# Performance work log

Hardware: AMD Instinct MI355X
Metric: run time of the kernel (lower is better)

## Reference

```python
import jax, jax.numpy as jnp
import numpy as np

B, T, C = 2, 2048, 1024
NUM_HEADS, QK_LEN, V_LEN = 16, 64, 64


def setup_inputs() -> dict:
    key = jax.random.key(0)
    ks = jax.random.split(key, 11)
    s = 0.02
    return {
        "Q": jax.random.normal(ks[0], (B, T, C), jnp.float32),
        "K": jax.random.normal(ks[1], (B, T, C), jnp.float32),
        "V": jax.random.normal(ks[2], (B, T, C), jnp.float32),
        # Linear weights stored as (in, out); y = x @ W + b
        "Wq": jax.random.normal(ks[3], (C, NUM_HEADS * QK_LEN), jnp.float32) * s,
        "bq": jnp.zeros((NUM_HEADS * QK_LEN,), jnp.float32),
        "Wk": jax.random.normal(ks[4], (C, NUM_HEADS * QK_LEN), jnp.float32) * s,
        "bk": jnp.zeros((NUM_HEADS * QK_LEN,), jnp.float32),
        "Wv": jax.random.normal(ks[5], (C, NUM_HEADS * V_LEN), jnp.float32) * s,
        "bv": jnp.zeros((NUM_HEADS * V_LEN,), jnp.float32),
        "Wo": jax.random.normal(ks[6], (NUM_HEADS * V_LEN, C), jnp.float32) * s,
        "bo": jnp.zeros((C,), jnp.float32),
    }


def _split_heads(x, n_heads, d):
    b, t, _ = x.shape
    return x.reshape(b, t, n_heads, d).transpose(0, 2, 1, 3)  # (B,H,T,d)


def reference(Q, K, V, Wq, bq, Wk, bk, Wv, bv, Wo, bo):
    q = _split_heads(Q @ Wq + bq, NUM_HEADS, QK_LEN)   # (B,H,T,dk)
    k = _split_heads(K @ Wk + bk, NUM_HEADS, QK_LEN)   # (B,H,T,dk)
    v = _split_heads(V @ Wv + bv, NUM_HEADS, V_LEN)    # (B,H,T,dv)

    scale = 1.0 / jnp.sqrt(jnp.asarray(QK_LEN, q.dtype))
    scores = jnp.einsum("bhqd,bhkd->bhqk", q, k) * scale  # (B,H,T,T)
    attn = jax.nn.softmax(scores, axis=-1)
    out = jnp.einsum("bhqk,bhkd->bhqd", attn, v)           # (B,H,T,dv)

    out = out.transpose(0, 2, 1, 3).reshape(Q.shape[0], Q.shape[1], NUM_HEADS * V_LEN)
    return out @ Wo + bo
```

## Files before the change

kernel.cpp:

```cpp
#include <hip/hip_runtime.h>
#include <hip/hip_bf16.h>
#include <math.h>

constexpr int B = 2, T = 2048, C = 1024, H = 16, D = 64;
constexpr int M = B * T;
constexpr float SCALE_L2E = 0.125f * 1.4426950408889634f;

typedef __attribute__((ext_vector_type(8))) short s16x8;
typedef __attribute__((ext_vector_type(4))) short s16x4;
typedef __attribute__((ext_vector_type(4))) float fv4;

typedef unsigned short ushort_t;

static __device__ __forceinline__ ushort_t f2bf(float x) {
    union { float f; unsigned u; } c; c.f = x;
    unsigned u = c.u + 0x7FFFu + ((c.u >> 16) & 1u);
    return (ushort_t)(u >> 16);
}

static __device__ __forceinline__ int cvt_pk_bf16(float lo, float hi) {
    int r;
    asm("v_cvt_pk_bf16_f32 %0, %1, %2" : "=v"(r) : "v"(lo), "v"(hi));
    return r;
}

#define GLDS(gp, lp) __builtin_amdgcn_global_load_lds( \
    (const __attribute__((address_space(1))) void*)(gp), \
    (__attribute__((address_space(3))) void*)(lp), 16, 0, 0)

__global__ __launch_bounds__(256) void prep(
    const float* __restrict__ Q, const float* __restrict__ K,
    const float* __restrict__ V,
    const float* __restrict__ W0, const float* __restrict__ W1,
    const float* __restrict__ W2, const float* __restrict__ W3,
    ushort_t* __restrict__ dst, ushort_t* __restrict__ Wt)
{
    __shared__ ushort_t tile[64][72];
    const int tid = threadIdx.x;

    if (blockIdx.x < 6144) {
        size_t e = ((size_t)blockIdx.x * 256 + tid) * 8;
        const float* src;
        size_t base;
        if (e < (size_t)M * C)          { src = Q; base = 0; }
        else if (e < 2 * (size_t)M * C) { src = K; base = (size_t)M * C; }
        else                            { src = V; base = 2 * (size_t)M * C; }
        const float* p = src + (e - base);
        float4 a = *(const float4*)p;
        float4 b = *(const float4*)(p + 4);
        union { s16x8 v; int i[4]; } o;
        o.i[0] = cvt_pk_bf16(a.x, a.y);
        o.i[1] = cvt_pk_bf16(a.z, a.w);
        o.i[2] = cvt_pk_bf16(b.x, b.y);
        o.i[3] = cvt_pk_bf16(b.z, b.w);
        *(s16x8*)(dst + e) = o.v;
        return;
    }

    const int idx = blockIdx.x - 6144;
    const int s = idx >> 8;
    const float* W = (s == 0) ? W0 : (s == 1) ? W1 : (s == 2) ? W2 : W3;
    const int k0 = (idx & 15) * 64, n0 = ((idx >> 4) & 15) * 64;
#pragma unroll
    for (int it = 0; it < 4; it++) {
        int f = it * 256 + tid;
        int r = f >> 4, c4 = (f & 15) * 4;
        float4 x = *(const float4*)(W + (size_t)(k0 + r) * C + n0 + c4);
        *(int*)&tile[r][c4]     = cvt_pk_bf16(x.x, x.y);
        *(int*)&tile[r][c4 + 2] = cvt_pk_bf16(x.z, x.w);
    }
    __syncthreads();
#pragma unroll
    for (int it = 0; it < 4; it++) {
        int f = it * 256 + tid;
        int rr = f >> 4, c4 = (f & 15) * 4;
        union { s16x4 v; ushort_t u[4]; } u;
#pragma unroll
        for (int j = 0; j < 4; j++) u.u[j] = tile[c4 + j][rr];
        *(s16x4*)(Wt + (size_t)(s * 1024 + n0 + rr) * 1024 + k0 + c4) = u.v;
    }
}

__global__ __launch_bounds__(256) void gemm_qkv(
    const ushort_t* __restrict__ qkv, const ushort_t* __restrict__ Wt,
    const float* __restrict__ bq, const float* __restrict__ bk,
    const float* __restrict__ bv,
    ushort_t* __restrict__ qw, ushort_t* __restrict__ kw,
    ushort_t* __restrict__ vt)
{
    __shared__ ushort_t As[2][128 * 32];
    __shared__ ushort_t Bs[2][128 * 32];

    const int tid = threadIdx.x;
    const int w = tid >> 6, lane = tid & 63;
    const int quad = lane >> 4, lc = lane & 15;
    const int wm = w & 1, wn = w >> 1;

    const int nt = blockIdx.x;
    const int m0 = blockIdx.y * 128;
    const int s = nt >> 3;
    const int nsec0 = (nt & 7) * 128;

    const ushort_t* Abase = qkv + (size_t)s * M * C;
    const ushort_t* Btbase = Wt + (size_t)nt * 128 * 1024;

    const int srow = (w << 4) + (lane >> 2);
    const int ske  = (lane & 3) * 8;

    fv4 acc[4][4] = {};

    auto stage = [&](int k0, int buf) {
#pragma unroll
        for (int i = 0; i < 2; i++) {
            int row = i * 64 + srow;
            GLDS(Abase + (size_t)(m0 + row) * 1024 + k0 + ske,
                 As[buf] + i * 2048 + w * 512);
            GLDS(Btbase + (size_t)row * 1024 + k0 + ske,
                 Bs[buf] + i * 2048 + w * 512);
        }
    };

    stage(0, 0);
    __syncthreads();

    for (int k0 = 0; k0 < 1024; k0 += 32) {
        const int cur = (k0 >> 5) & 1;
        if (k0 + 32 < 1024) stage(k0 + 32, cur ^ 1);

        s16x8 af[4], bf[4];
#pragma unroll
        for (int ms = 0; ms < 4; ms++)
            af[ms] = *(const s16x8*)(As[cur] + (wm * 64 + ms * 16 + lc) * 32 + quad * 8);
#pragma unroll
        for (int ns = 0; ns < 4; ns++)
            bf[ns] = *(const s16x8*)(Bs[cur] + (wn * 64 + ns * 16 + lc) * 32 + quad * 8);
#pragma unroll
        for (int ms = 0; ms < 4; ms++)
#pragma unroll
            for (int ns = 0; ns < 4; ns++)
                acc[ms][ns] = __builtin_amdgcn_mfma_f32_16x16x32_bf16(
                    af[ms], bf[ns], acc[ms][ns], 0, 0, 0);
        __syncthreads();
    }

    if (s == 2) {
#pragma unroll
        for (int ns = 0; ns < 4; ns++) {
            const int nl = nsec0 + wn * 64 + ns * 16 + lc;
            const float bias = bv[nl];
            const int h_ = nl >> 6, d_ = nl & 63;
#pragma unroll
            for (int ms = 0; ms < 4; ms++) {
                int m = m0 + wm * 64 + ms * 16 + quad * 4;
                int b_ = m >> 11, t_ = m & (T - 1);
                size_t row = (size_t)(b_ * H + h_) * 64 + d_;
                union { s16x4 v; int i[2]; } u;
                u.i[0] = cvt_pk_bf16(acc[ms][ns][0] + bias, acc[ms][ns][1] + bias);
                u.i[1] = cvt_pk_bf16(acc[ms][ns][2] + bias, acc[ms][ns][3] + bias);
                *(s16x4*)(vt + row * T + t_) = u.v;
            }
        }
        return;
    }

    const float* biasp = (s == 0) ? bq : bk;
    const float premul = (s == 0) ? SCALE_L2E : 1.0f;
    ushort_t* outp = (s == 0) ? qw : kw;

#pragma unroll
    for (int ns = 0; ns < 4; ns++) {
        const int nl = nsec0 + wn * 64 + ns * 16 + lc;
        const float bias = biasp[nl];
        const int h_ = nl >> 6, d_ = nl & 63;
#pragma unroll
        for (int ms = 0; ms < 4; ms++) {
#pragma unroll
            for (int r = 0; r < 4; r++) {
                int m = m0 + wm * 64 + ms * 16 + quad * 4 + r;
                float val = (acc[ms][ns][r] + bias) * premul;
                int b_ = m >> 11, t_ = m & (T - 1);
                size_t bh = (size_t)(b_ * H + h_);
                outp[((bh * T + t_) << 6) + d_] = f2bf(val);
            }
        }
    }
}

__global__ __launch_bounds__(256) void gemm_final(
    const ushort_t* __restrict__ A, const ushort_t* __restrict__ Wot,
    const float* __restrict__ bo, float* __restrict__ out)
{
    __shared__ ushort_t As[2][128 * 32];
    __shared__ ushort_t Bs[2][64 * 32];

    const int tid = threadIdx.x;
    const int w = tid >> 6, lane = tid & 63;
    const int quad = lane >> 4, lc = lane & 15;
    const int wm = w & 1, wn = w >> 1;

    const int n0 = blockIdx.x * 64;
    const int m0 = blockIdx.y * 128;

    const int srow = (w << 4) + (lane >> 2);
    const int ske  = (lane & 3) * 8;

    fv4 acc[4][2] = {};

    auto stage = [&](int k0, int buf) {
        GLDS(A + (size_t)(m0 + srow) * 1024 + k0 + ske,      As[buf] + w * 512);
        GLDS(A + (size_t)(m0 + 64 + srow) * 1024 + k0 + ske, As[buf] + 2048 + w * 512);
        GLDS(Wot + (size_t)(n0 + srow) * 1024 + k0 + ske,    Bs[buf] + w * 512);
    };

    stage(0, 0);
    __syncthreads();

    for (int k0 = 0; k0 < 1024; k0 += 32) {
        const int cur = (k0 >> 5) & 1;
        if (k0 + 32 < 1024) stage(k0 + 32, cur ^ 1);

        s16x8 af[4], bf[2];
#pragma unroll
        for (int ms = 0; ms < 4; ms++)
            af[ms] = *(const s16x8*)(As[cur] + (wm * 64 + ms * 16 + lc) * 32 + quad * 8);
#pragma unroll
        for (int ns = 0; ns < 2; ns++)
            bf[ns] = *(const s16x8*)(Bs[cur] + (wn * 32 + ns * 16 + lc) * 32 + quad * 8);
#pragma unroll
        for (int ms = 0; ms < 4; ms++)
#pragma unroll
            for (int ns = 0; ns < 2; ns++)
                acc[ms][ns] = __builtin_amdgcn_mfma_f32_16x16x32_bf16(
                    af[ms], bf[ns], acc[ms][ns], 0, 0, 0);
        __syncthreads();
    }

#pragma unroll
    for (int ns = 0; ns < 2; ns++) {
        const int n = n0 + wn * 32 + ns * 16 + lc;
        const float bias = bo[n];
#pragma unroll
        for (int ms = 0; ms < 4; ms++) {
#pragma unroll
            for (int r = 0; r < 4; r++) {
                int m = m0 + wm * 64 + ms * 16 + quad * 4 + r;
                out[(size_t)m * 1024 + n] = acc[ms][ns][r] + bias;
            }
        }
    }
}

__global__ __launch_bounds__(256, 4) void attn(
    const ushort_t* __restrict__ q, const ushort_t* __restrict__ k,
    const ushort_t* __restrict__ vT, ushort_t* __restrict__ o)
{
    __shared__ alignas(16) ushort_t ks[2][64 * 64];
    __shared__ alignas(16) ushort_t vs[2][64 * 64];

    const int tid = threadIdx.x;
    const int w = tid >> 6, lane = tid & 63;
    const int quad = lane >> 4, lc = lane & 15;
    const int cs = lc & 7;
    const int qsub = w & 1, ksub = w >> 1;

    const int id = blockIdx.y * 32 + blockIdx.x;
    const int qt = (id >> 3) & 31;
    const int bh = (id & 7) * 4 + (id >> 8);

    s16x8 aq[2][2];
    const ushort_t* qb = q + ((size_t)bh * T + qt * 64 + qsub * 32) * D;
#pragma unroll
    for (int j = 0; j < 2; j++)
#pragma unroll
        for (int h = 0; h < 2; h++)
            aq[j][h] = *(const s16x8*)(qb + (size_t)(j * 16 + lc) * D + h * 32 + quad * 8);

    fv4 accO[2][4] = {};
    float psum[2] = {0.f, 0.f};

    const ushort_t* kb0 = k + (size_t)bh * T * D;
    const ushort_t* vb0 = vT + (size_t)bh * D * T;

    const int sr8 = lane >> 3;
    const int sch = (lane & 7) ^ sr8;

    auto stage = [&](int kt, int buf) {
#pragma unroll
        for (int i = 0; i < 2; i++) {
            const int r = w * 16 + i * 8 + sr8;
            GLDS(kb0 + (size_t)(kt * 64 + r) * 64 + sch * 8,
                 ks[buf] + (w * 16 + i * 8) * 64);
            GLDS(vb0 + (size_t)r * T + kt * 64 + sch * 8,
                 vs[buf] + (w * 16 + i * 8) * 64);
        }
    };

    stage(0, 0);
    __syncthreads();

    for (int kt = 0; kt < T / 64; kt++) {
        const int cur = kt & 1;
        if (kt + 1 < T / 64) stage(kt + 1, cur ^ 1);

        fv4 accST[2][2] = {};
        __builtin_amdgcn_s_setprio(1);
#pragma unroll
        for (int t4k = 0; t4k < 2; t4k++) {
            const int row = ksub * 32 + t4k * 16 + lc;
            s16x8 ak0 = *(const s16x8*)(ks[cur] + row * 64 + ((quad ^ cs) << 3));
            s16x8 ak1 = *(const s16x8*)(ks[cur] + row * 64 + (((quad + 4) ^ cs) << 3));
#pragma unroll
            for (int j = 0; j < 2; j++) {
                accST[j][t4k] = __builtin_amdgcn_mfma_f32_16x16x32_bf16(
                    ak0, aq[j][0], accST[j][t4k], 0, 0, 0);
                accST[j][t4k] = __builtin_amdgcn_mfma_f32_16x16x32_bf16(
                    ak1, aq[j][1], accST[j][t4k], 0, 0, 0);
            }
        }
        __builtin_amdgcn_s_setprio(0);

        s16x8 av[4];
#pragma unroll
        for (int t4v = 0; t4v < 4; t4v++) {
            const int row = t4v * 16 + lc;
            av[t4v] = *(const s16x8*)(vs[cur] + row * 64 + (((ksub * 4 + quad) ^ cs) << 3));
        }

#pragma unroll
        for (int j = 0; j < 2; j++) {
            float p0 = __builtin_amdgcn_exp2f(accST[j][0][0]);
            float p1 = __builtin_amdgcn_exp2f(accST[j][0][1]);
            float p2 = __builtin_amdgcn_exp2f(accST[j][0][2]);
            float p3 = __builtin_amdgcn_exp2f(accST[j][0][3]);
            float p4 = __builtin_amdgcn_exp2f(accST[j][1][0]);
            float p5 = __builtin_amdgcn_exp2f(accST[j][1][1]);
            float p6 = __builtin_amdgcn_exp2f(accST[j][1][2]);
            float p7 = __builtin_amdgcn_exp2f(accST[j][1][3]);
            psum[j] += ((p0 + p1) + (p2 + p3)) + ((p4 + p5) + (p6 + p7));

            int W00 = cvt_pk_bf16(p0, p1);
            int W01 = cvt_pk_bf16(p2, p3);
            int W10 = cvt_pk_bf16(p4, p5);
            int W11 = cvt_pk_bf16(p6, p7);
            asm("v_permlane32_swap_b32 %0, %1" : "+v"(W00), "+v"(W10));
            asm("v_permlane16_swap_b32 %0, %1" : "+v"(W00), "+v"(W10));
            asm("v_permlane32_swap_b32 %0, %1" : "+v"(W01), "+v"(W11));
            asm("v_permlane16_swap_b32 %0, %1" : "+v"(W01), "+v"(W11));

            union { int i[4]; s16x8 v; } pbu;
            pbu.i[0] = W00; pbu.i[1] = W01; pbu.i[2] = W10; pbu.i[3] = W11;

            __builtin_amdgcn_s_setprio(1);
#pragma unroll
            for (int t4v = 0; t4v < 4; t4v++)
                accO[j][t4v] = __builtin_amdgcn_mfma_f32_16x16x32_bf16(
                    av[t4v], pbu.v, accO[j][t4v], 0, 0, 0);
            __builtin_amdgcn_s_setprio(0);
        }

        __syncthreads();
    }

#pragma unroll
    for (int j = 0; j < 2; j++) {
        psum[j] += __shfl_xor(psum[j], 16);
        psum[j] += __shfl_xor(psum[j], 32);
    }

    float* sc = (float*)&ks[0][0];
#pragma unroll
    for (int c = 0; c < 4; c++) {
        const int j = c >> 1, tv = (c & 1) * 2;
        __syncthreads();
        if (ksub == 1) {
            *(fv4*)(sc + ((qsub * 64 + lane) * 8))     = accO[j][tv];
            *(fv4*)(sc + ((qsub * 64 + lane) * 8 + 4)) = accO[j][tv + 1];
        }
        __syncthreads();
        if (ksub == 0) {
            accO[j][tv]     += *(fv4*)(sc + ((qsub * 64 + lane) * 8));
            accO[j][tv + 1] += *(fv4*)(sc + ((qsub * 64 + lane) * 8 + 4));
        }
    }
    __syncthreads();
    if (ksub == 1) {
        sc[(qsub * 64 + lane) * 2]     = psum[0];
        sc[(qsub * 64 + lane) * 2 + 1] = psum[1];
    }
    __syncthreads();
    if (ksub == 0) {
        psum[0] += sc[(qsub * 64 + lane) * 2];
        psum[1] += sc[(qsub * 64 + lane) * 2 + 1];

        const int b_ = bh >> 4, h_ = bh & 15;
#pragma unroll
        for (int j = 0; j < 2; j++) {
            float inv = 1.0f / psum[j];
            int row = qt * 64 + qsub * 32 + j * 16 + lc;
            ushort_t* op = o + ((size_t)b_ * T + row) * C + h_ * 64;
#pragma unroll
            for (int t4v = 0; t4v < 4; t4v++) {
                union { s16x4 v; int i[2]; } u;
                u.i[0] = cvt_pk_bf16(accO[j][t4v][0] * inv, accO[j][t4v][1] * inv);
                u.i[1] = cvt_pk_bf16(accO[j][t4v][2] * inv, accO[j][t4v][3] * inv);
                *(s16x4*)(op + t4v * 16 + quad * 4) = u.v;
            }
        }
    }
}

extern "C" void kernel_launch(void* const* d_in, const int* in_sizes, int n_in,
                              void* d_out, int out_size, void* d_ws, size_t ws_size,
                              hipStream_t stream)
{
    const float* Q  = (const float*)d_in[0];
    const float* K  = (const float*)d_in[1];
    const float* V  = (const float*)d_in[2];
    const float* Wq = (const float*)d_in[3];
    const float* bq = (const float*)d_in[4];
    const float* Wk = (const float*)d_in[5];
    const float* bk = (const float*)d_in[6];
    const float* Wv = (const float*)d_in[7];
    const float* bv = (const float*)d_in[8];
    const float* Wo = (const float*)d_in[9];
    const float* bo = (const float*)d_in[10];
    float* out = (float*)d_out;

    ushort_t* qkvbf = (ushort_t*)d_ws;
    ushort_t* Wt = qkvbf + (size_t)3 * M * C;
    ushort_t* qw = Wt + (size_t)4096 * 1024;
    ushort_t* kw = qw + (size_t)M * C;
    ushort_t* vt = kw + (size_t)M * C;
    ushort_t* ow = qkvbf;
    ushort_t* Wot = Wt + (size_t)3072 * 1024;

    dim3 blk(256);
    prep<<<dim3(7168), blk, 0, stream>>>(Q, K, V, Wq, Wk, Wv, Wo, qkvbf, Wt);
    gemm_qkv<<<dim3(24, 32), blk, 0, stream>>>(qkvbf, Wt, bq, bk, bv, qw, kw, vt);
    attn<<<dim3(T / 64, B * H), blk, 0, stream>>>(qw, kw, vt, ow);
    gemm_final<<<dim3(16, 32), blk, 0, stream>>>(ow, Wot, bo, out);
}
```

Before: 248.8 us.

## Remap GEMM tiles per XCD and stage V-transpose output through LDS

Both projection GEMMs now remap the linear block index so that consecutive blocks dispatched to the same XCD share the same M rows of A, which should improve L2 reuse across the chiplets' separate caches. The V-output epilogue of the QKV GEMM now writes the accumulator tile into shared memory (padded rows) and then emits coalesced 16-byte row stores of the transposed V, replacing scattered 8-byte stores. The remap assumes round-robin block-to-XCD dispatch, and the epilogue adds an extra barrier and reuses the A/B staging LDS.

```diff
diff --git a/kernel.cpp b/kernel.cpp
--- a/kernel.cpp
+++ b/kernel.cpp
@@ -88,17 +88,22 @@
     ushort_t* __restrict__ qw, ushort_t* __restrict__ kw,
     ushort_t* __restrict__ vt)
 {
-    __shared__ ushort_t As[2][128 * 32];
-    __shared__ ushort_t Bs[2][128 * 32];
+    __shared__ ushort_t sm[17408];
+    ushort_t* As0 = sm;
+    ushort_t* Bs0 = sm + 8192;
 
     const int tid = threadIdx.x;
     const int w = tid >> 6, lane = tid & 63;
     const int quad = lane >> 4, lc = lane & 15;
     const int wm = w & 1, wn = w >> 1;
 
-    const int nt = blockIdx.x;
-    const int m0 = blockIdx.y * 128;
-    const int s = nt >> 3;
+    const int lin = blockIdx.y * 24 + blockIdx.x;
+    const int xcd = lin % 8;
+    const int i_ = lin / 8;
+    const int s = i_ >> 5;
+    const int r_ = i_ & 31;
+    const int m0 = (xcd * 4 + (r_ >> 3)) * 128;
+    const int nt = s * 8 + (r_ & 7);
     const int nsec0 = (nt & 7) * 128;
 
     const ushort_t* Abase = qkv + (size_t)s * M * C;
@@ -114,9 +119,9 @@
         for (int i = 0; i < 2; i++) {
             int row = i * 64 + srow;
             GLDS(Abase + (size_t)(m0 + row) * 1024 + k0 + ske,
-                 As[buf] + i * 2048 + w * 512);
+                 As0 + buf * 4096 + i * 2048 + w * 512);
             GLDS(Btbase + (size_t)row * 1024 + k0 + ske,
-                 Bs[buf] + i * 2048 + w * 512);
+                 Bs0 + buf * 4096 + i * 2048 + w * 512);
         }
     };
 
@@ -130,10 +135,10 @@
         s16x8 af[4], bf[4];
 #pragma unroll
         for (int ms = 0; ms < 4; ms++)
-            af[ms] = *(const s16x8*)(As[cur] + (wm * 64 + ms * 16 + lc) * 32 + quad * 8);
+            af[ms] = *(const s16x8*)(As0 + cur * 4096 + (wm * 64 + ms * 16 + lc) * 32 + quad * 8);
 #pragma unroll
         for (int ns = 0; ns < 4; ns++)
-            bf[ns] = *(const s16x8*)(Bs[cur] + (wn * 64 + ns * 16 + lc) * 32 + quad * 8);
+            bf[ns] = *(const s16x8*)(Bs0 + cur * 4096 + (wn * 64 + ns * 16 + lc) * 32 + quad * 8);
 #pragma unroll
         for (int ms = 0; ms < 4; ms++)
 #pragma unroll
@@ -144,21 +149,30 @@
     }
 
     if (s == 2) {
+        ushort_t* tp = sm;
 #pragma unroll
         for (int ns = 0; ns < 4; ns++) {
-            const int nl = nsec0 + wn * 64 + ns * 16 + lc;
-            const float bias = bv[nl];
-            const int h_ = nl >> 6, d_ = nl & 63;
+            const int nl = wn * 64 + ns * 16 + lc;
+            const float bias = bv[nsec0 + nl];
 #pragma unroll
             for (int ms = 0; ms < 4; ms++) {
-                int m = m0 + wm * 64 + ms * 16 + quad * 4;
-                int b_ = m >> 11, t_ = m & (T - 1);
-                size_t row = (size_t)(b_ * H + h_) * 64 + d_;
-                union { s16x4 v; int i[2]; } u;
-                u.i[0] = cvt_pk_bf16(acc[ms][ns][0] + bias, acc[ms][ns][1] + bias);
-                u.i[1] = cvt_pk_bf16(acc[ms][ns][2] + bias, acc[ms][ns][3] + bias);
-                *(s16x4*)(vt + row * T + t_) = u.v;
+                const int ml = wm * 64 + ms * 16 + quad * 4;
+                union { s16x4 v; int i2[2]; } u;
+                u.i2[0] = cvt_pk_bf16(acc[ms][ns][0] + bias, acc[ms][ns][1] + bias);
+                u.i2[1] = cvt_pk_bf16(acc[ms][ns][2] + bias, acc[ms][ns][3] + bias);
+                *(s16x4*)&tp[nl * 136 + ml] = u.v;
             }
+        }
+        __syncthreads();
+        const int b_ = m0 >> 11, t0 = m0 & 2047;
+#pragma unroll
+        for (int it = 0; it < 8; it++) {
+            const int row = it * 16 + (tid >> 4);
+            const int ch = tid & 15;
+            const int n = nsec0 + row;
+            const int h_ = n >> 6, d_ = n & 63;
+            s16x8 v8 = *(const s16x8*)&tp[row * 136 + ch * 8];
+            *(s16x8*)(vt + ((size_t)(b_ * H + h_) * 64 + d_) * T + t0 + ch * 8) = v8;
         }
         return;
     }
@@ -198,8 +212,11 @@
     const int quad = lane >> 4, lc = lane & 15;
     const int wm = w & 1, wn = w >> 1;
 
-    const int n0 = blockIdx.x * 64;
-    const int m0 = blockIdx.y * 128;
+    const int lin = blockIdx.y * 16 + blockIdx.x;
+    const int xcd = lin & 7;
+    const int i_ = lin >> 3;
+    const int m0 = (xcd * 4 + (i_ >> 4)) * 128;
+    const int n0 = (i_ & 15) * 64;
 
     const int srow = (w << 4) + (lane >> 2);
     const int ske  = (lane & 3) * 8;
```

Result: faster. 221.9 us (-10.8%).
